# Optimization experiments

Measured on AMD Instinct MI355X. Metric: run time of the kernel, lower is better.

Reference implementation:

```python
import jax, jax.numpy as jnp
import numpy as np

B, T, C, H = 2, 2048, 1024, 16
HD = C // H          # head dim = 64
HD2 = HD // 2        # rotary half = 32


def setup_inputs() -> dict:
    key = jax.random.key(0)
    k0, k1, k2 = jax.random.split(key, 3)
    x = jax.random.normal(k0, (B, T, C), jnp.float32)
    Wqkv = jax.random.normal(k1, (C, 3 * C), jnp.float32) * (1.0 / np.sqrt(C))
    bqkv = jnp.zeros((3 * C,), jnp.float32)
    Wproj = jax.random.normal(k2, (C, C), jnp.float32) * (1.0 / np.sqrt(C))
    bproj = jnp.zeros((C,), jnp.float32)
    # standard rotary frequencies: theta_i = 10000^{-2i/hd}
    inv_freq = 1.0 / (10000.0 ** (jnp.arange(0, HD, 2, dtype=jnp.float32) / HD))
    angles = jnp.arange(T, dtype=jnp.float32)[:, None] * inv_freq[None, :]  # (T, HD2)
    return {
        "x": x,
        "freqs_cos": jnp.cos(angles),
        "freqs_sin": jnp.sin(angles),
        "Wqkv": Wqkv,
        "bqkv": bqkv,
        "Wproj": Wproj,
        "bproj": bproj,
    }


def _rope(u, cos, sin):
    # u: (B, T, H, HD); half-split pairing: (u[i], u[i + HD/2]) form a complex pair
    u1, u2 = u[..., :HD2], u[..., HD2:]
    c = cos[None, :, None, :]  # (1, T, 1, HD2)
    s = sin[None, :, None, :]
    return jnp.concatenate([u1 * c - u2 * s, u1 * s + u2 * c], axis=-1)


def reference(x, freqs_cos, freqs_sin, Wqkv, bqkv, Wproj, bproj):
    Bc, Tc, Cc = x.shape
    qkv = x @ Wqkv + bqkv                      # (B, T, 3C)
    q, k, v = jnp.split(qkv, 3, axis=-1)
    q = q.reshape(Bc, Tc, H, HD)
    k = k.reshape(Bc, Tc, H, HD)
    v = v.reshape(Bc, Tc, H, HD)
    q = _rope(q, freqs_cos, freqs_sin)
    k = _rope(k, freqs_cos, freqs_sin)
    scale = 1.0 / np.sqrt(HD)
    scores = jnp.einsum("bthd,bshd->bhts", q, k) * scale  # (B, H, T, T)
    causal = jnp.tril(jnp.ones((Tc, Tc), dtype=bool))
    scores = jnp.where(causal[None, None], scores, jnp.finfo(scores.dtype).min)
    p = jax.nn.softmax(scores, axis=-1)
    y = jnp.einsum("bhts,bshd->bthd", p, v).reshape(Bc, Tc, Cc)
    return y @ Wproj + bproj
```

## Files before the change

### kernel.cpp

```cpp
#include <hip/hip_runtime.h>
#include <hip/hip_bf16.h>
#include <cstdint>
#include <cmath>

typedef __bf16 bf16_t;
typedef __attribute__((ext_vector_type(8))) __bf16 bf16x8;
typedef __attribute__((ext_vector_type(4))) float f32x4;

#define LOG2E 1.4426950408889634f

constexpr int B_ = 2, T_ = 2048, C_ = 1024, H_ = 16, HD_ = 64, HD2_ = 32;
constexpr int M_ = B_ * T_;

static __device__ __forceinline__ f32x4 mfma16(bf16x8 a, bf16x8 b, f32x4 c) {
    return __builtin_amdgcn_mfma_f32_16x16x32_bf16(a, b, c, 0, 0, 0);
}

#define GLL(gp, lp)                                                          \
    __builtin_amdgcn_global_load_lds(                                        \
        (const __attribute__((address_space(1))) void*)(gp),                 \
        (__attribute__((address_space(3))) void*)(lp), 16, 0, 0)

__global__ void prep(const float* __restrict__ x, bf16_t* __restrict__ xb,
                     const float* __restrict__ Wqkv, bf16_t* __restrict__ wqkvT,
                     const float* __restrict__ Wproj, bf16_t* __restrict__ wprojT) {
    __shared__ float tile[32][33];
    const int bid = blockIdx.x, tid = threadIdx.x;
    if (bid < 4096) {
        int i = bid * 256 + tid;
        float4 v = ((const float4*)x)[i];
        bf16_t o[4] = {(bf16_t)v.x, (bf16_t)v.y, (bf16_t)v.z, (bf16_t)v.w};
        *(uint64_t*)(xb + (size_t)i * 4) = *(uint64_t*)o;
        return;
    }
    const float* W;
    bf16_t* WT;
    int K, N, nb, kb;
    if (bid < 4096 + 3072) {
        int t = bid - 4096;
        W = Wqkv; WT = wqkvT; K = C_; N = 3 * C_;
        nb = (t % 96) * 32; kb = (t / 96) * 32;
    } else {
        int t = bid - 7168;
        W = Wproj; WT = wprojT; K = C_; N = C_;
        nb = (t & 31) * 32; kb = (t >> 5) * 32;
    }
    int tx = tid & 31, ty = tid >> 5;
    for (int i = ty; i < 32; i += 8)
        tile[i][tx] = W[(size_t)(kb + i) * N + nb + tx];
    __syncthreads();
    for (int i = ty; i < 32; i += 8)
        WT[(size_t)(nb + i) * K + kb + tx] = (bf16_t)tile[tx][i];
}

template <int MODE>
__global__ __launch_bounds__(256, 3) void gemm128(
    const bf16_t* __restrict__ A, const bf16_t* __restrict__ BT, const float* __restrict__ bias,
    int N, int K,
    bf16_t* __restrict__ Qb, bf16_t* __restrict__ Kb, bf16_t* __restrict__ VTb,
    const float* __restrict__ cosT, const float* __restrict__ sinT, float* __restrict__ out) {
    constexpr int NT = (MODE == 1) ? 2 : 4;
    constexpr int BPARTS = (MODE == 1) ? 2 : 4;
    __shared__ alignas(16) bf16_t As[128 * 64];
    __shared__ alignas(16) bf16_t Bs[32 * BPARTS * 64];
    const int tid = threadIdx.x;
    const int w = tid >> 6, lane = tid & 63;
    const int quad = lane >> 4, r = lane & 15;
    const int wm = (w >> 1) * 64, wn = (w & 1) * (16 * NT);
    const int bid = blockIdx.x;
    const int xcd = bid & 7, s = bid >> 3;
    int mb, nb;
    if (MODE == 0) {
        mb = (((xcd >> 1) << 3) + (s & 7)) << 7;
        nb = (((xcd & 1) * 12 + (s >> 3))) << 7;
    } else {
        mb = (((xcd >> 1) << 3) + (s & 7)) << 7;
        nb = (((xcd & 1) << 3) + (s >> 3)) << 6;
    }
    const int srow = tid >> 3, schunk = tid & 7;
    const int csw = (schunk ^ (srow & 7)) * 8;
    const int koff0 = (quad ^ (r & 7)) * 8;
    const int koff1 = ((quad + 4) ^ (r & 7)) * 8;

    f32x4 acc[4][NT] = {};

    const bf16_t* gA[4];
    const bf16_t* gB[BPARTS];
#pragma unroll
    for (int p = 0; p < 4; p++) gA[p] = A + (size_t)(mb + p * 32 + srow) * K + csw;
#pragma unroll
    for (int p = 0; p < BPARTS; p++) gB[p] = BT + (size_t)(nb + p * 32 + srow) * K + csw;

    for (int k0 = 0; k0 < K; k0 += 64) {
        __syncthreads();
#pragma unroll
        for (int p = 0; p < 4; p++) GLL(gA[p] + k0, As + p * 2048 + tid * 8);
#pragma unroll
        for (int p = 0; p < BPARTS; p++) GLL(gB[p] + k0, Bs + p * 2048 + tid * 8);
        __syncthreads();
#pragma unroll
        for (int h = 0; h < 2; h++) {
            const int ko = h ? koff1 : koff0;
            bf16x8 af[4], bfr[NT];
#pragma unroll
            for (int i = 0; i < 4; i++) af[i] = *(const bf16x8*)(As + (wm + i * 16 + r) * 64 + ko);
#pragma unroll
            for (int j = 0; j < NT; j++) bfr[j] = *(const bf16x8*)(Bs + (wn + j * 16 + r) * 64 + ko);
#pragma unroll
            for (int i = 0; i < 4; i++)
#pragma unroll
                for (int j = 0; j < NT; j++) acc[i][j] = mfma16(af[i], bfr[j], acc[i][j]);
        }
    }

    if (MODE == 0) {
        const int col_base = nb + wn;
        const int region = col_base >> 10;
        const int h = (col_base & 1023) >> 6;
        const float qscale = 0.125f * LOG2E;
        if (region < 2) {
#pragma unroll
            for (int i = 0; i < 4; i++) {
#pragma unroll
                for (int g = 0; g < 4; g++) {
                    int m = mb + wm + i * 16 + quad * 4 + g;
                    int b = m >> 11, t = m & (T_ - 1);
                    bf16_t* dst = (region == 0 ? Qb : Kb) + ((size_t)((b * H_ + h) * T_ + t)) * 64;
                    int tw = t & 7;
#pragma unroll
                    for (int j = 0; j < 2; j++) {
                        int d = j * 16 + r;
                        float u1 = acc[i][j][g] + bias[col_base + d];
                        float u2 = acc[i][j + 2][g] + bias[col_base + d + 32];
                        float c = cosT[t * HD2_ + d], s2 = sinT[t * HD2_ + d];
                        float o1 = u1 * c - u2 * s2;
                        float o2 = u1 * s2 + u2 * c;
                        if (region == 0) {
                            dst[d] = (bf16_t)(o1 * qscale);
                            dst[d + 32] = (bf16_t)(o2 * qscale);
                        } else {
                            dst[((((d >> 3) ^ tw)) << 3) | (d & 7)] = (bf16_t)o1;
                            dst[(((((d + 32) >> 3) ^ tw)) << 3) | (d & 7)] = (bf16_t)o2;
                        }
                    }
                }
            }
        } else {
#pragma unroll
            for (int i = 0; i < 4; i++) {
                int m0 = mb + wm + i * 16 + quad * 4;
                int b = m0 >> 11, t0 = m0 & (T_ - 1);
                bf16_t* base = VTb + (size_t)(b * H_ + h) * 64 * T_;
#pragma unroll
                for (int j = 0; j < 4; j++) {
                    int d = j * 16 + r;
                    float bb = bias[col_base + d];
                    bf16_t pk[4];
#pragma unroll
                    for (int g = 0; g < 4; g++) pk[g] = (bf16_t)(acc[i][j][g] + bb);
                    int c = (((t0 >> 3) & 7) ^ (d & 7));
                    int tsw = (t0 & ~63) | (c << 3) | (t0 & 7);
                    *(uint64_t*)(base + (size_t)d * T_ + tsw) = *(uint64_t*)pk;
                }
            }
        }
    } else {
#pragma unroll
        for (int i = 0; i < 4; i++)
#pragma unroll
            for (int g = 0; g < 4; g++) {
                int m = mb + wm + i * 16 + quad * 4 + g;
#pragma unroll
                for (int j = 0; j < NT; j++) {
                    int col = nb + wn + j * 16 + r;
                    out[(size_t)m * N + col] = acc[i][j][g] + bias[col];
                }
            }
    }
}

__global__ __launch_bounds__(512, 4) void attn64(
    const bf16_t* __restrict__ Qb, const bf16_t* __restrict__ Kb,
    const bf16_t* __restrict__ VTb, bf16_t* __restrict__ att) {
    __shared__ alignas(16) bf16_t Ks[2][2][4096];
    __shared__ alignas(16) bf16_t Vs[2][2][4096];
    __shared__ alignas(16) bf16_t Ps[8][1024];
    const int tid = threadIdx.x;
    const int w = tid >> 6, lane = tid & 63;
    const int grp = w >> 2, wq = w & 3;
    const int quad = lane >> 4, r = lane & 15;
    const int id = blockIdx.x;
    const int t = 31 - (id >> 5);
    const int bh = id & 31;
    const int ntiles = t + 1, nstages = (t + 2) >> 1;
    const size_t kbase = (size_t)bh * T_ * 64;
    const size_t vbase = (size_t)bh * 64 * T_;
    bf16_t* Pw = &Ps[w][0];
    const int srow = tid >> 3, schunk = tid & 7;
    const int koff0 = ((quad ^ (r & 7)) * 8);
    const int koff1 = (((quad + 4) ^ (r & 7)) * 8);

    const int qrow = t * 64 + wq * 16 + r;
    bf16x8 qf0 = *(const bf16x8*)(Qb + kbase + (size_t)qrow * 64 + quad * 8);
    bf16x8 qf1 = *(const bf16x8*)(Qb + kbase + (size_t)qrow * 64 + 32 + quad * 8);

    f32x4 oacc[4] = {};
    float l = 0.f;

    {
        const bf16_t* kg = Kb + kbase + (size_t)srow * 64 + schunk * 8;
        GLL(kg, &Ks[0][0][0] + tid * 8);
        const bf16_t* vg = VTb + vbase + (size_t)srow * T_ + schunk * 8;
        GLL(vg, &Vs[0][0][0] + tid * 8);
        if (1 < ntiles) {
            GLL(kg + 64 * 64, &Ks[0][1][0] + tid * 8);
            GLL(vg + 64, &Vs[0][1][0] + tid * 8);
        }
    }
    for (int s = 0; s < nstages; s++) {
        const int cur = s & 1;
        __syncthreads();
        if (s + 1 < nstages) {
            const int ja = 2 * (s + 1);
            const bf16_t* kg = Kb + kbase + (size_t)(ja * 64 + srow) * 64 + schunk * 8;
            const bf16_t* vg = VTb + vbase + (size_t)srow * T_ + ja * 64 + schunk * 8;
            GLL(kg, &Ks[cur ^ 1][0][0] + tid * 8);
            GLL(vg, &Vs[cur ^ 1][0][0] + tid * 8);
            if (ja + 1 < ntiles) {
                GLL(kg + 64 * 64, &Ks[cur ^ 1][1][0] + tid * 8);
                GLL(vg + 64, &Vs[cur ^ 1][1][0] + tid * 8);
            }
        }
        const int jt = 2 * s + grp;
        if (jt < ntiles) {
            const bf16_t* Kt = &Ks[cur][grp][0];
            const bf16_t* Vt = &Vs[cur][grp][0];
            f32x4 sc[4];
#pragma unroll
            for (int m0 = 0; m0 < 4; m0++) {
                const bf16_t* kp = Kt + (m0 * 16 + r) * 64;
                bf16x8 kf0 = *(const bf16x8*)(kp + koff0);
                bf16x8 kf1 = *(const bf16x8*)(kp + koff1);
                f32x4 z = {0.f, 0.f, 0.f, 0.f};
                z = mfma16(kf0, qf0, z);
                z = mfma16(kf1, qf1, z);
                sc[m0] = z;
            }
            if (jt == t) {
                const int j0 = jt * 64;
#pragma unroll
                for (int m0 = 0; m0 < 4; m0++) {
                    int kvb = j0 + m0 * 16 + quad * 4;
#pragma unroll
                    for (int g = 0; g < 4; g++)
                        if (kvb + g > qrow) sc[m0][g] = -INFINITY;
                }
            }
            float rs = 0.f;
#pragma unroll
            for (int m0 = 0; m0 < 4; m0++)
#pragma unroll
                for (int g = 0; g < 4; g++) {
                    float pp = __builtin_amdgcn_exp2f(sc[m0][g]);
                    sc[m0][g] = pp;
                    rs += pp;
                }
            l += rs;
#pragma unroll
            for (int m0 = 0; m0 < 4; m0++) {
                bf16_t hq[4];
#pragma unroll
                for (int g = 0; g < 4; g++) hq[g] = (bf16_t)sc[m0][g];
                int elem = (m0 >> 1) * 512 + (((m0 & 1) * 2 + (quad >> 1)) * 16 + r) * 8 + (quad & 1) * 4;
                *(uint64_t*)(Pw + elem) = *(uint64_t*)hq;
            }
            __builtin_amdgcn_wave_barrier();
            bf16x8 pf0 = *(const bf16x8*)(Pw + lane * 8);
            bf16x8 pf1 = *(const bf16x8*)(Pw + 512 + lane * 8);
#pragma unroll
            for (int d0 = 0; d0 < 4; d0++) {
                const bf16_t* vp = Vt + (d0 * 16 + r) * 64;
                bf16x8 vf0 = *(const bf16x8*)(vp + koff0);
                bf16x8 vf1 = *(const bf16x8*)(vp + koff1);
                oacc[d0] = mfma16(vf0, pf0, oacc[d0]);
                oacc[d0] = mfma16(vf1, pf1, oacc[d0]);
            }
        }
    }
    l += __shfl_xor(l, 16);
    l += __shfl_xor(l, 32);
    __syncthreads();
    float* Co = (float*)&Ks[0][0][0];
    float* Cl = (float*)&Vs[0][0][0];
    if (grp == 1) {
#pragma unroll
        for (int d0 = 0; d0 < 4; d0++)
            *(f32x4*)(Co + wq * 1024 + r * 64 + d0 * 16 + quad * 4) = oacc[d0];
        if (quad == 0) Cl[wq * 16 + r] = l;
    }
    __syncthreads();
    if (grp == 0) {
        float inv = 1.f / (l + Cl[wq * 16 + r]);
        const int b = bh >> 4, h = bh & 15;
        bf16_t* dst = att + ((size_t)(b * T_ + qrow)) * 1024 + h * 64;
#pragma unroll
        for (int d0 = 0; d0 < 4; d0++) {
            f32x4 o1 = *(const f32x4*)(Co + wq * 1024 + r * 64 + d0 * 16 + quad * 4);
            bf16_t hh[4];
#pragma unroll
            for (int g = 0; g < 4; g++)
                hh[g] = (bf16_t)((oacc[d0][g] + o1[g]) * inv);
            *(uint64_t*)(dst + d0 * 16 + quad * 4) = *(uint64_t*)hh;
        }
    }
}

extern "C" void kernel_launch(void* const* d_in, const int* in_sizes, int n_in,
                              void* d_out, int out_size, void* d_ws, size_t ws_size,
                              hipStream_t stream) {
    const float* x = (const float*)d_in[0];
    const float* fcos = (const float*)d_in[1];
    const float* fsin = (const float*)d_in[2];
    const float* Wqkv = (const float*)d_in[3];
    const float* bqkv = (const float*)d_in[4];
    const float* Wproj = (const float*)d_in[5];
    const float* bproj = (const float*)d_in[6];
    float* out = (float*)d_out;

    uint8_t* p = (uint8_t*)d_ws;
    size_t need = 0;
    auto take = [&](size_t bytes) {
        void* q = p;
        size_t pad = (bytes + 255) & ~(size_t)255;
        p += pad;
        need += pad;
        return q;
    };
    bf16_t* xb = (bf16_t*)take((size_t)M_ * C_ * 2);
    bf16_t* wqkvT = (bf16_t*)take((size_t)3 * C_ * C_ * 2);
    bf16_t* wprojT = (bf16_t*)take((size_t)C_ * C_ * 2);
    bf16_t* Qb = (bf16_t*)take((size_t)B_ * H_ * T_ * 64 * 2);
    bf16_t* Kb = (bf16_t*)take((size_t)B_ * H_ * T_ * 64 * 2);
    bf16_t* VTb = (bf16_t*)take((size_t)B_ * H_ * 64 * T_ * 2);
    bf16_t* attb = (bf16_t*)take((size_t)M_ * C_ * 2);
    if (ws_size < need) return;

    prep<<<8192, 256, 0, stream>>>(x, xb, Wqkv, wqkvT, Wproj, wprojT);

    gemm128<0><<<dim3(768), 256, 0, stream>>>(
        xb, wqkvT, bqkv, 3 * C_, C_, Qb, Kb, VTb, fcos, fsin, nullptr);

    attn64<<<dim3(1024), 512, 0, stream>>>(Qb, Kb, VTb, attb);

    gemm128<1><<<dim3(512), 256, 0, stream>>>(
        attb, wprojT, bproj, C_, C_, nullptr, nullptr, nullptr, nullptr, nullptr, out);
}
```

Before: 174.0 us.

## Widen attention query tile to 128 rows so each K/V tile is reused twice

The attention kernel now gives each block 128 query rows instead of 64, and each wave handles two 16-row query fragments against every K/V tile loaded into LDS. This halves the K/V global-to-LDS traffic per query and the block count, and the triangular iteration always processes tile pairs, which drops the per-tile bounds checks. It also adds s_setprio around the MFMA sections. In exchange it doubles accumulator registers and P scratch space, lowers the occupancy hint from 4 to 2 blocks, and uses 512 blocks, so load balance across CUs is coarser.

```diff
diff --git a/kernel.cpp b/kernel.cpp
--- a/kernel.cpp
+++ b/kernel.cpp
@@ -179,20 +179,20 @@
     }
 }
 
-__global__ __launch_bounds__(512, 4) void attn64(
+__global__ __launch_bounds__(512, 2) void attn128(
     const bf16_t* __restrict__ Qb, const bf16_t* __restrict__ Kb,
     const bf16_t* __restrict__ VTb, bf16_t* __restrict__ att) {
     __shared__ alignas(16) bf16_t Ks[2][2][4096];
     __shared__ alignas(16) bf16_t Vs[2][2][4096];
-    __shared__ alignas(16) bf16_t Ps[8][1024];
+    __shared__ alignas(16) bf16_t Ps[8][2048];
     const int tid = threadIdx.x;
     const int w = tid >> 6, lane = tid & 63;
     const int grp = w >> 2, wq = w & 3;
     const int quad = lane >> 4, r = lane & 15;
     const int id = blockIdx.x;
-    const int t = 31 - (id >> 5);
+    const int pp = 15 - (id >> 5);
     const int bh = id & 31;
-    const int ntiles = t + 1, nstages = (t + 2) >> 1;
+    const int ntiles = 2 * pp + 2, nstages = pp + 1;
     const size_t kbase = (size_t)bh * T_ * 64;
     const size_t vbase = (size_t)bh * 64 * T_;
     bf16_t* Pw = &Ps[w][0];
@@ -200,22 +200,23 @@
     const int koff0 = ((quad ^ (r & 7)) * 8);
     const int koff1 = (((quad + 4) ^ (r & 7)) * 8);
 
-    const int qrow = t * 64 + wq * 16 + r;
-    bf16x8 qf0 = *(const bf16x8*)(Qb + kbase + (size_t)qrow * 64 + quad * 8);
-    bf16x8 qf1 = *(const bf16x8*)(Qb + kbase + (size_t)qrow * 64 + 32 + quad * 8);
-
-    f32x4 oacc[4] = {};
-    float l = 0.f;
+    const int qbase = pp * 128 + wq * 32;
+    const int qrow0 = qbase + r, qrow1 = qbase + 16 + r;
+    bf16x8 qf00 = *(const bf16x8*)(Qb + kbase + (size_t)qrow0 * 64 + quad * 8);
+    bf16x8 qf01 = *(const bf16x8*)(Qb + kbase + (size_t)qrow0 * 64 + 32 + quad * 8);
+    bf16x8 qf10 = *(const bf16x8*)(Qb + kbase + (size_t)qrow1 * 64 + quad * 8);
+    bf16x8 qf11 = *(const bf16x8*)(Qb + kbase + (size_t)qrow1 * 64 + 32 + quad * 8);
+
+    f32x4 oacc[4][2] = {};
+    float l0 = 0.f, l1 = 0.f;
 
     {
         const bf16_t* kg = Kb + kbase + (size_t)srow * 64 + schunk * 8;
+        const bf16_t* vg = VTb + vbase + (size_t)srow * T_ + schunk * 8;
         GLL(kg, &Ks[0][0][0] + tid * 8);
-        const bf16_t* vg = VTb + vbase + (size_t)srow * T_ + schunk * 8;
+        GLL(kg + 4096, &Ks[0][1][0] + tid * 8);
         GLL(vg, &Vs[0][0][0] + tid * 8);
-        if (1 < ntiles) {
-            GLL(kg + 64 * 64, &Ks[0][1][0] + tid * 8);
-            GLL(vg + 64, &Vs[0][1][0] + tid * 8);
-        }
+        GLL(vg + 64, &Vs[0][1][0] + tid * 8);
     }
     for (int s = 0; s < nstages; s++) {
         const int cur = s & 1;
@@ -225,92 +226,123 @@
             const bf16_t* kg = Kb + kbase + (size_t)(ja * 64 + srow) * 64 + schunk * 8;
             const bf16_t* vg = VTb + vbase + (size_t)srow * T_ + ja * 64 + schunk * 8;
             GLL(kg, &Ks[cur ^ 1][0][0] + tid * 8);
+            GLL(kg + 4096, &Ks[cur ^ 1][1][0] + tid * 8);
             GLL(vg, &Vs[cur ^ 1][0][0] + tid * 8);
-            if (ja + 1 < ntiles) {
-                GLL(kg + 64 * 64, &Ks[cur ^ 1][1][0] + tid * 8);
-                GLL(vg + 64, &Vs[cur ^ 1][1][0] + tid * 8);
-            }
+            GLL(vg + 64, &Vs[cur ^ 1][1][0] + tid * 8);
         }
         const int jt = 2 * s + grp;
-        if (jt < ntiles) {
-            const bf16_t* Kt = &Ks[cur][grp][0];
-            const bf16_t* Vt = &Vs[cur][grp][0];
-            f32x4 sc[4];
+        const bf16_t* Kt = &Ks[cur][grp][0];
+        const bf16_t* Vt = &Vs[cur][grp][0];
+        f32x4 sc[4][2];
+        __builtin_amdgcn_s_setprio(1);
+#pragma unroll
+        for (int m0 = 0; m0 < 4; m0++) {
+            const bf16_t* kp = Kt + (m0 * 16 + r) * 64;
+            bf16x8 kf0 = *(const bf16x8*)(kp + koff0);
+            bf16x8 kf1 = *(const bf16x8*)(kp + koff1);
+            f32x4 z0 = {0.f, 0.f, 0.f, 0.f};
+            z0 = mfma16(kf0, qf00, z0);
+            z0 = mfma16(kf1, qf01, z0);
+            sc[m0][0] = z0;
+            f32x4 z1 = {0.f, 0.f, 0.f, 0.f};
+            z1 = mfma16(kf0, qf10, z1);
+            z1 = mfma16(kf1, qf11, z1);
+            sc[m0][1] = z1;
+        }
+        __builtin_amdgcn_s_setprio(0);
+        if (s + 1 == nstages) {
+            const int j0 = jt * 64;
 #pragma unroll
             for (int m0 = 0; m0 < 4; m0++) {
-                const bf16_t* kp = Kt + (m0 * 16 + r) * 64;
-                bf16x8 kf0 = *(const bf16x8*)(kp + koff0);
-                bf16x8 kf1 = *(const bf16x8*)(kp + koff1);
-                f32x4 z = {0.f, 0.f, 0.f, 0.f};
-                z = mfma16(kf0, qf0, z);
-                z = mfma16(kf1, qf1, z);
-                sc[m0] = z;
-            }
-            if (jt == t) {
-                const int j0 = jt * 64;
-#pragma unroll
-                for (int m0 = 0; m0 < 4; m0++) {
-                    int kvb = j0 + m0 * 16 + quad * 4;
-#pragma unroll
-                    for (int g = 0; g < 4; g++)
-                        if (kvb + g > qrow) sc[m0][g] = -INFINITY;
+                int kvb = j0 + m0 * 16 + quad * 4;
+#pragma unroll
+                for (int g = 0; g < 4; g++) {
+                    if (kvb + g > qrow0) sc[m0][0][g] = -INFINITY;
+                    if (kvb + g > qrow1) sc[m0][1][g] = -INFINITY;
                 }
             }
-            float rs = 0.f;
-#pragma unroll
-            for (int m0 = 0; m0 < 4; m0++)
-#pragma unroll
-                for (int g = 0; g < 4; g++) {
-                    float pp = __builtin_amdgcn_exp2f(sc[m0][g]);
-                    sc[m0][g] = pp;
-                    rs += pp;
-                }
-            l += rs;
+        }
+        float rs0 = 0.f, rs1 = 0.f;
+#pragma unroll
+        for (int m0 = 0; m0 < 4; m0++)
+#pragma unroll
+            for (int g = 0; g < 4; g++) {
+                float p0 = __builtin_amdgcn_exp2f(sc[m0][0][g]);
+                float p1 = __builtin_amdgcn_exp2f(sc[m0][1][g]);
+                sc[m0][0][g] = p0;
+                sc[m0][1][g] = p1;
+                rs0 += p0;
+                rs1 += p1;
+            }
+        l0 += rs0;
+        l1 += rs1;
+#pragma unroll
+        for (int jq = 0; jq < 2; jq++)
 #pragma unroll
             for (int m0 = 0; m0 < 4; m0++) {
                 bf16_t hq[4];
 #pragma unroll
-                for (int g = 0; g < 4; g++) hq[g] = (bf16_t)sc[m0][g];
-                int elem = (m0 >> 1) * 512 + (((m0 & 1) * 2 + (quad >> 1)) * 16 + r) * 8 + (quad & 1) * 4;
+                for (int g = 0; g < 4; g++) hq[g] = (bf16_t)sc[m0][jq][g];
+                int elem = jq * 1024 + (m0 >> 1) * 512 +
+                           (((m0 & 1) * 2 + (quad >> 1)) * 16 + r) * 8 + (quad & 1) * 4;
                 *(uint64_t*)(Pw + elem) = *(uint64_t*)hq;
             }
-            __builtin_amdgcn_wave_barrier();
-            bf16x8 pf0 = *(const bf16x8*)(Pw + lane * 8);
-            bf16x8 pf1 = *(const bf16x8*)(Pw + 512 + lane * 8);
-#pragma unroll
-            for (int d0 = 0; d0 < 4; d0++) {
-                const bf16_t* vp = Vt + (d0 * 16 + r) * 64;
-                bf16x8 vf0 = *(const bf16x8*)(vp + koff0);
-                bf16x8 vf1 = *(const bf16x8*)(vp + koff1);
-                oacc[d0] = mfma16(vf0, pf0, oacc[d0]);
-                oacc[d0] = mfma16(vf1, pf1, oacc[d0]);
-            }
-        }
-    }
-    l += __shfl_xor(l, 16);
-    l += __shfl_xor(l, 32);
+        __builtin_amdgcn_wave_barrier();
+        bf16x8 pf00 = *(const bf16x8*)(Pw + lane * 8);
+        bf16x8 pf01 = *(const bf16x8*)(Pw + 512 + lane * 8);
+        bf16x8 pf10 = *(const bf16x8*)(Pw + 1024 + lane * 8);
+        bf16x8 pf11 = *(const bf16x8*)(Pw + 1536 + lane * 8);
+        __builtin_amdgcn_s_setprio(1);
+#pragma unroll
+        for (int d0 = 0; d0 < 4; d0++) {
+            const bf16_t* vp = Vt + (d0 * 16 + r) * 64;
+            bf16x8 vf0 = *(const bf16x8*)(vp + koff0);
+            bf16x8 vf1 = *(const bf16x8*)(vp + koff1);
+            oacc[d0][0] = mfma16(vf0, pf00, oacc[d0][0]);
+            oacc[d0][0] = mfma16(vf1, pf01, oacc[d0][0]);
+            oacc[d0][1] = mfma16(vf0, pf10, oacc[d0][1]);
+            oacc[d0][1] = mfma16(vf1, pf11, oacc[d0][1]);
+        }
+        __builtin_amdgcn_s_setprio(0);
+    }
+    l0 += __shfl_xor(l0, 16);
+    l0 += __shfl_xor(l0, 32);
+    l1 += __shfl_xor(l1, 16);
+    l1 += __shfl_xor(l1, 32);
     __syncthreads();
     float* Co = (float*)&Ks[0][0][0];
     float* Cl = (float*)&Vs[0][0][0];
     if (grp == 1) {
 #pragma unroll
-        for (int d0 = 0; d0 < 4; d0++)
-            *(f32x4*)(Co + wq * 1024 + r * 64 + d0 * 16 + quad * 4) = oacc[d0];
-        if (quad == 0) Cl[wq * 16 + r] = l;
+        for (int jq = 0; jq < 2; jq++)
+#pragma unroll
+            for (int d0 = 0; d0 < 4; d0++)
+                *(f32x4*)(Co + ((wq * 2 + jq) * 16 + r) * 64 + d0 * 16 + quad * 4) =
+                    oacc[d0][jq];
+        if (quad == 0) {
+            Cl[(wq * 2) * 16 + r] = l0;
+            Cl[(wq * 2 + 1) * 16 + r] = l1;
+        }
     }
     __syncthreads();
     if (grp == 0) {
-        float inv = 1.f / (l + Cl[wq * 16 + r]);
         const int b = bh >> 4, h = bh & 15;
-        bf16_t* dst = att + ((size_t)(b * T_ + qrow)) * 1024 + h * 64;
-#pragma unroll
-        for (int d0 = 0; d0 < 4; d0++) {
-            f32x4 o1 = *(const f32x4*)(Co + wq * 1024 + r * 64 + d0 * 16 + quad * 4);
-            bf16_t hh[4];
-#pragma unroll
-            for (int g = 0; g < 4; g++)
-                hh[g] = (bf16_t)((oacc[d0][g] + o1[g]) * inv);
-            *(uint64_t*)(dst + d0 * 16 + quad * 4) = *(uint64_t*)hh;
+#pragma unroll
+        for (int jq = 0; jq < 2; jq++) {
+            float lsum = (jq ? l1 : l0) + Cl[(wq * 2 + jq) * 16 + r];
+            float inv = 1.f / lsum;
+            const int qrow = qbase + jq * 16 + r;
+            bf16_t* dst = att + ((size_t)(b * T_ + qrow)) * 1024 + h * 64;
+#pragma unroll
+            for (int d0 = 0; d0 < 4; d0++) {
+                f32x4 o1 =
+                    *(const f32x4*)(Co + ((wq * 2 + jq) * 16 + r) * 64 + d0 * 16 + quad * 4);
+                bf16_t hh[4];
+#pragma unroll
+                for (int g = 0; g < 4; g++)
+                    hh[g] = (bf16_t)((oacc[d0][jq][g] + o1[g]) * inv);
+                *(uint64_t*)(dst + d0 * 16 + quad * 4) = *(uint64_t*)hh;
+            }
         }
     }
 }
@@ -350,7 +382,7 @@
     gemm128<0><<<dim3(768), 256, 0, stream>>>(
         xb, wqkvT, bqkv, 3 * C_, C_, Qb, Kb, VTb, fcos, fsin, nullptr);
 
-    attn64<<<dim3(1024), 512, 0, stream>>>(Qb, Kb, VTb, attb);
+    attn128<<<dim3(512), 512, 0, stream>>>(Qb, Kb, VTb, attb);
 
     gemm128<1><<<dim3(512), 256, 0, stream>>>(
         attb, wprojT, bproj, C_, C_, nullptr, nullptr, nullptr, nullptr, nullptr, out);
```

New measurement: 178.4 us. 1.03x slower.
